# Kernel tuning notes

Measured on AMD Instinct MI355X. Metric: run time of the kernel, lower is better.

Reference implementation:

```python
import jax, jax.numpy as jnp
import numpy as np

HIDDEN = 2048
HEADS = 16
HEAD_DIM = HIDDEN // HEADS  # 128
B, S = 2, 2048
SCALE = 1.0 / np.sqrt(HEAD_DIM)


def setup_inputs() -> dict:
    key = jax.random.key(0)
    ks = jax.random.split(key, 9)
    x = jax.random.normal(ks[0], (B, S, HIDDEN), dtype=jnp.float32)
    # causal mask, broadcastable to [B, 1(group), H, S, S]
    mask = jnp.tril(jnp.ones((S, S), dtype=bool))[None, None, None, :, :]
    mask = jnp.broadcast_to(mask, (B, 1, 1, S, S))
    s = 0.02
    Wq = jax.random.normal(ks[1], (HIDDEN, HIDDEN), dtype=jnp.float32) * s
    bq = jnp.zeros((HIDDEN,), dtype=jnp.float32)
    Wk = jax.random.normal(ks[2], (HIDDEN, HEAD_DIM), dtype=jnp.float32) * s
    bk = jnp.zeros((HEAD_DIM,), dtype=jnp.float32)
    Wv = jax.random.normal(ks[3], (HIDDEN, HEAD_DIM), dtype=jnp.float32) * s
    bv = jnp.zeros((HEAD_DIM,), dtype=jnp.float32)
    Wo = jax.random.normal(ks[4], (HIDDEN, HIDDEN), dtype=jnp.float32) * s
    bo = jnp.zeros((HIDDEN,), dtype=jnp.float32)
    return {"x": x, "mask": mask, "Wq": Wq, "bq": bq, "Wk": Wk, "bk": bk,
            "Wv": Wv, "bv": bv, "Wo": Wo, "bo": bo}


def reference(x, mask, Wq, bq, Wk, bk, Wv, bv, Wo, bo):
    b, s, _ = x.shape
    q = (x @ Wq + bq).reshape(b, s, HEADS, HEAD_DIM)   # [b,s,h,d]
    k = x @ Wk + bk                                    # [b,t,d] single shared KV head
    v = x @ Wv + bv                                    # [b,t,d]
    # scores: [b, h, s, t]; add group dim to match mask [b,1,h,s,t]
    scores = jnp.einsum('bshd,btd->bhst', q, k) * SCALE
    scores = scores[:, None]                            # [b,1,h,s,t]
    scores = jnp.where(mask, scores, jnp.float32(-jnp.inf))
    att = jax.nn.softmax(scores, axis=-1)[:, 0]         # [b,h,s,t] (dropout eval = identity)
    out = jnp.einsum('bhst,btd->bshd', att, v).reshape(b, s, HIDDEN)
    return out @ Wo + bo
```

## Files before the change

### kernel.cpp

```cpp
#include <hip/hip_runtime.h>


#define HIDDEN 2048
#define NHEADS 16
#define HDIM 128
#define BATCH 2
#define SEQ 2048
#define SCALE_L2E 0.1275258653864023f

typedef __attribute__((ext_vector_type(8))) short bfrag;
typedef __attribute__((ext_vector_type(4))) float facc;

__device__ __forceinline__ unsigned short f2bf(float f) {
  unsigned int u = __float_as_uint(f);
  u += 0x7fffu + ((u >> 16) & 1u);
  return (unsigned short)(u >> 16);
}

__device__ __forceinline__ unsigned int cvt_pk_bf16(float lo, float hi) {
  unsigned int r;
  asm("v_cvt_pk_bf16_f32 %0, %1, %2" : "=v"(r) : "v"(lo), "v"(hi));
  return r;
}

__device__ __forceinline__ void gl_lds16(const void* g, void* l) {
  __builtin_amdgcn_global_load_lds(
      (const __attribute__((address_space(1))) void*)g,
      (__attribute__((address_space(3))) void*)l, 16, 0, 0);
}

__global__ __launch_bounds__(256) void cvt_bf16(const float* __restrict__ in,
                                                unsigned int* __restrict__ out, int n4) {
  int i = blockIdx.x * 256 + threadIdx.x;
  if (i >= n4) return;
  float4 v = ((const float4*)in)[i];
  uint2 o = {cvt_pk_bf16(v.x, v.y), cvt_pk_bf16(v.z, v.w)};
  ((uint2*)out)[i] = o;
}

__global__ __launch_bounds__(256) void transpose_cvt2(const float* __restrict__ W0,
                                                      short* __restrict__ T0,
                                                      const float* __restrict__ W1,
                                                      short* __restrict__ T1,
                                                      int K, int N) {
  const float* W = blockIdx.z ? W1 : W0;
  short* WT = blockIdx.z ? T1 : T0;
  __shared__ float t[32][33];
  int tx = threadIdx.x & 31, ty = threadIdx.x >> 5;
  int n0 = blockIdx.x * 32, k0 = blockIdx.y * 32;
#pragma unroll
  for (int j = 0; j < 4; ++j)
    t[ty + j * 8][tx] = W[(size_t)(k0 + ty + j * 8) * N + n0 + tx];
  __syncthreads();
#pragma unroll
  for (int j = 0; j < 4; ++j)
    WT[(size_t)(n0 + ty + j * 8) * K + k0 + tx] = (short)f2bf(t[tx][ty + j * 8]);
}

#define GEMM_STAGE8(buf, kt, A, BT, Kdim)                                      \
  _Pragma("unroll") for (int it_ = 0; it_ < 2; ++it_) {                        \
    int bc = (w * 2 + it_) * 64;                                               \
    int C = bc + l;                                                            \
    int row = C >> 3, c = C & 7;                                               \
    int gofs = (kt) * 64 + ((c ^ (row & 7)) << 3);                             \
    gl_lds16((A) + (size_t)(m0 + row) * (Kdim) + gofs, &Al[buf][bc * 8]);      \
    gl_lds16((BT) + (size_t)(n0 + row) * (Kdim) + gofs, &Bl[buf][bc * 8]);     \
  }

#define GEMM_PIPE_LOOP8(A, BT, Kdim)                                           \
  facc acc[2][4] = {};                                                         \
  const int nkt = (Kdim) >> 6;                                                 \
  GEMM_STAGE8(0, 0, A, BT, Kdim)                                               \
  __syncthreads();                                                             \
  for (int kt = 0; kt < nkt; ++kt) {                                           \
    const int cur = kt & 1;                                                    \
    if (kt + 1 < nkt) { GEMM_STAGE8(cur ^ 1, kt + 1, A, BT, Kdim) }            \
    __builtin_amdgcn_s_setprio(1);                                             \
    _Pragma("unroll") for (int ks = 0; ks < 2; ++ks) {                         \
      bfrag af[2], bf[4];                                                      \
      _Pragma("unroll") for (int mt = 0; mt < 2; ++mt) {                       \
        int row = wm * 32 + mt * 16 + l15;                                     \
        int c = ks * 4 + l4;                                                   \
        af[mt] = *(const bfrag*)&Al[cur][row * 64 + ((c ^ (row & 7)) << 3)];   \
      }                                                                        \
      _Pragma("unroll") for (int nt = 0; nt < 4; ++nt) {                       \
        int row = wn * 64 + nt * 16 + l15;                                     \
        int c = ks * 4 + l4;                                                   \
        bf[nt] = *(const bfrag*)&Bl[cur][row * 64 + ((c ^ (row & 7)) << 3)];   \
      }                                                                        \
      _Pragma("unroll") for (int mt = 0; mt < 2; ++mt)                         \
          _Pragma("unroll") for (int nt = 0; nt < 4; ++nt)                     \
              acc[mt][nt] = __builtin_amdgcn_mfma_f32_16x16x32_bf16(           \
                  af[mt], bf[nt], acc[mt][nt], 0, 0, 0);                       \
    }                                                                          \
    __builtin_amdgcn_s_setprio(0);                                             \
    __syncthreads();                                                           \
  }

__global__ __launch_bounds__(512, 4) void gemm_qkv(const short* __restrict__ A,
                                                   const short* __restrict__ BT,
                                                   const float* __restrict__ bq,
                                                   const float* __restrict__ bk,
                                                   const float* __restrict__ bv,
                                                   unsigned short* __restrict__ Qb,
                                                   unsigned short* __restrict__ Kb,
                                                   unsigned short* __restrict__ Vtb,
                                                   int M, int K) {
  __shared__ __align__(16) short Al[2][128 * 64];
  __shared__ __align__(16) short Bl[2][128 * 64];
  const int tid = threadIdx.x;
  const int w = tid >> 6, l = tid & 63;
  const int wm = w >> 1, wn = w & 1;
  const int l15 = l & 15, l4 = l >> 4;
  const int m0 = blockIdx.x * 128, n0 = blockIdx.y * 128;
  GEMM_PIPE_LOOP8(A, BT, K)
#pragma unroll
  for (int mt = 0; mt < 2; ++mt) {
#pragma unroll
    for (int nt = 0; nt < 4; ++nt) {
#pragma unroll
      for (int r = 0; r < 4; ++r) {
        int row = m0 + wm * 32 + mt * 16 + l4 * 4 + r;
        int col = n0 + wn * 64 + nt * 16 + l15;
        float v = acc[mt][nt][r];
        if (col < HIDDEN) {
          Qb[(size_t)row * HIDDEN + col] = f2bf(v + bq[col]);
        } else if (col < HIDDEN + HDIM) {
          int lc = col - HIDDEN;
          Kb[(size_t)row * HDIM + lc] = f2bf(v + bk[lc]);
        } else {
          int lc = col - HIDDEN - HDIM;
          Vtb[(size_t)lc * M + row] = f2bf(v + bv[lc]);
        }
      }
    }
  }
}

__global__ __launch_bounds__(512, 4) void gemm_out(const short* __restrict__ A,
                                                   const short* __restrict__ BT,
                                                   const float* __restrict__ bias,
                                                   float* __restrict__ Cout,
                                                   int M, int N, int K) {
  __shared__ __align__(16) short Al[2][128 * 64];
  __shared__ __align__(16) short Bl[2][128 * 64];
  const int tid = threadIdx.x;
  const int w = tid >> 6, l = tid & 63;
  const int wm = w >> 1, wn = w & 1;
  const int l15 = l & 15, l4 = l >> 4;
  const int m0 = blockIdx.x * 128, n0 = blockIdx.y * 128;
  GEMM_PIPE_LOOP8(A, BT, K)
#pragma unroll
  for (int mt = 0; mt < 2; ++mt)
#pragma unroll
    for (int nt = 0; nt < 4; ++nt)
#pragma unroll
      for (int r = 0; r < 4; ++r) {
        int row = m0 + wm * 32 + mt * 16 + l4 * 4 + r;
        int col = n0 + wn * 64 + nt * 16 + l15;
        Cout[(size_t)row * N + col] = acc[mt][nt][r] + bias[col];
      }
}

__global__ __launch_bounds__(256, 2) void attn_kernel(const short* __restrict__ Q,
                                                      const short* __restrict__ Kg,
                                                      const short* __restrict__ Vt,
                                                      unsigned short* __restrict__ O) {
  __shared__ __align__(16) short Kl[2][64 * 128];
  __shared__ __align__(16) short Vl[2][128 * 64];
  __shared__ __align__(16) char Pl[4][2048];
  const int tid = threadIdx.x;
  const int w = tid >> 6, l = tid & 63;
  const int l15 = l & 15, l4 = l >> 4;
  const int h = blockIdx.y, b = blockIdx.z;

#define STAGE_KV(buf, t)                                                            \
  do {                                                                              \
    const int kv0_ = (t) << 6;                                                      \
    _Pragma("unroll") for (int it = 0; it < 4; ++it) {                              \
      int bc = (w * 4 + it) * 64;                                                   \
      int C = bc + l;                                                               \
      int key = C >> 4, c = C & 15;                                                 \
      gl_lds16(Kg + (size_t)(b * SEQ + kv0_ + key) * HDIM + ((c ^ (key & 7)) << 3), \
               &Kl[buf][bc * 8]);                                                   \
    }                                                                               \
    _Pragma("unroll") for (int it = 0; it < 4; ++it) {                              \
      int bc = (w * 4 + it) * 64;                                                   \
      int C = bc + l;                                                               \
      int d = C >> 3, c = C & 7;                                                    \
      gl_lds16(Vt + (size_t)d * (BATCH * SEQ) + b * SEQ + kv0_ + ((c ^ (d & 7)) << 3), \
               &Vl[buf][bc * 8]);                                                   \
    }                                                                               \
  } while (0)

  for (int pass = 0; pass < 2; ++pass) {
    const int qtile = (pass == 0) ? (int)blockIdx.x : 31 - (int)blockIdx.x;
    const int q0 = qtile * 64;
    const int qw = q0 + w * 16;

    bfrag aq[4];
#pragma unroll
    for (int kk = 0; kk < 4; ++kk)
      aq[kk] = *(const bfrag*)(Q + (size_t)(b * SEQ + qw + l15) * HIDDEN +
                               h * HDIM + kk * 32 + l4 * 8);

    facc accO[8] = {};
    float mrow = -INFINITY, lrow = 0.f;
    const int nkv = qtile + 1;

    STAGE_KV(0, 0);
    __syncthreads();

    for (int t = 0; t < nkv; ++t) {
      const int cur = t & 1;
      if (t + 1 < nkv) STAGE_KV(cur ^ 1, t + 1);
      const int kv0 = t << 6;

      facc sac[4] = {};
      __builtin_amdgcn_s_setprio(1);
#pragma unroll
      for (int kk = 0; kk < 4; ++kk) {
        int c = kk * 4 + l4;
#pragma unroll
        for (int kt = 0; kt < 4; ++kt) {
          int key = kt * 16 + l15;
          bfrag ak = *(const bfrag*)&Kl[cur][key * 128 + ((c ^ (key & 7)) << 3)];
          sac[kt] = __builtin_amdgcn_mfma_f32_16x16x32_bf16(ak, aq[kk], sac[kt], 0, 0, 0);
        }
      }
      __builtin_amdgcn_s_setprio(0);

      const int qg = qw + l15;
      const bool needmask = (kv0 + 63 > qw);
      float p[4][4];
      float mt = -INFINITY;
#pragma unroll
      for (int kt = 0; kt < 4; ++kt)
#pragma unroll
        for (int r = 0; r < 4; ++r) {
          float v = sac[kt][r] * SCALE_L2E;
          if (needmask) {
            int keyg = kv0 + kt * 16 + l4 * 4 + r;
            v = (keyg <= qg) ? v : -INFINITY;
          }
          p[kt][r] = v;
          mt = fmaxf(mt, v);
        }
      mt = fmaxf(mt, __shfl_xor(mt, 16));
      mt = fmaxf(mt, __shfl_xor(mt, 32));
      float mn = fmaxf(mrow, mt);
      float f = exp2f(mrow - mn);
      mrow = mn;
      float ps = 0.f;
#pragma unroll
      for (int kt = 0; kt < 4; ++kt)
#pragma unroll
        for (int r = 0; r < 4; ++r) {
          p[kt][r] = exp2f(p[kt][r] - mn);
          ps += p[kt][r];
        }
      ps += __shfl_xor(ps, 16);
      ps += __shfl_xor(ps, 32);
      lrow = lrow * f + ps;
      float fr[4];
#pragma unroll
      for (int r = 0; r < 4; ++r) fr[r] = __shfl(f, l4 * 4 + r);

      char* pw = &Pl[w][0];
#pragma unroll
      for (int kt = 0; kt < 4; ++kt)
#pragma unroll
        for (int rp = 0; rp < 2; ++rp) {
          unsigned int u = cvt_pk_bf16(p[kt][2 * rp], p[kt][2 * rp + 1]);
          int byte = (l15 * 128 + (kt * 16 + l4 * 4 + 2 * rp) * 2) ^ ((l15 & 7) << 4);
          *(unsigned int*)(pw + byte) = u;
        }
#pragma unroll
      for (int nt = 0; nt < 8; ++nt)
#pragma unroll
        for (int r = 0; r < 4; ++r) accO[nt][r] *= fr[r];

      __builtin_amdgcn_s_setprio(1);
#pragma unroll
      for (int kc = 0; kc < 2; ++kc) {
        bfrag pa = *(const bfrag*)(&Pl[w][0] +
                                   ((l15 * 128 + (kc * 32 + l4 * 8) * 2) ^ ((l15 & 7) << 4)));
#pragma unroll
        for (int nt = 0; nt < 8; ++nt) {
          int d = nt * 16 + l15;
          int cslot = (kc * 4 + l4) ^ (d & 7);
          bfrag bv = *(const bfrag*)&Vl[cur][d * 64 + (cslot << 3)];
          accO[nt] = __builtin_amdgcn_mfma_f32_16x16x32_bf16(pa, bv, accO[nt], 0, 0, 0);
        }
      }
      __builtin_amdgcn_s_setprio(0);
      __syncthreads();
    }

    float inv = 1.f / lrow;
#pragma unroll
    for (int r = 0; r < 4; ++r) {
      float invr = __shfl(inv, l4 * 4 + r);
      int row = qw + l4 * 4 + r;
#pragma unroll
      for (int nt = 0; nt < 8; ++nt)
        O[(size_t)(b * SEQ + row) * HIDDEN + h * HDIM + nt * 16 + l15] =
            f2bf(accO[nt][r] * invr);
    }
  }
#undef STAGE_KV
}

extern "C" void kernel_launch(void* const* d_in, const int* in_sizes, int n_in,
                              void* d_out, int out_size, void* d_ws, size_t ws_size,
                              hipStream_t stream) {
  const float* x = (const float*)d_in[0];
  const float* Wq = (const float*)d_in[2];
  const float* bq = (const float*)d_in[3];
  const float* Wk = (const float*)d_in[4];
  const float* bk = (const float*)d_in[5];
  const float* Wv = (const float*)d_in[6];
  const float* bv = (const float*)d_in[7];
  const float* Wo = (const float*)d_in[8];
  const float* bo = (const float*)d_in[9];
  float* out = (float*)d_out;

  const size_t MS = (size_t)BATCH * SEQ;
  char* ws = (char*)d_ws;
  short* xb = (short*)ws;      ws += MS * HIDDEN * 2;
  short* WqkvT = (short*)ws;   ws += (size_t)(HIDDEN + 2 * HDIM) * HIDDEN * 2;
  short* WoT = (short*)ws;     ws += (size_t)HIDDEN * HIDDEN * 2;
  short* Qb = (short*)ws;      ws += MS * HIDDEN * 2;
  short* Kb = (short*)ws;      ws += MS * HDIM * 2;
  short* Vtb = (short*)ws;     ws += (size_t)HDIM * MS * 2;
  short* Ab = (short*)ws;      ws += MS * HIDDEN * 2;

  cvt_bf16<<<(int)(MS * HIDDEN / 4 / 256), 256, 0, stream>>>(
      x, (unsigned int*)xb, (int)(MS * HIDDEN / 4));
  transpose_cvt2<<<dim3(HIDDEN / 32, HIDDEN / 32, 2), 256, 0, stream>>>(
      Wq, WqkvT, Wo, WoT, HIDDEN, HIDDEN);
  transpose_cvt2<<<dim3(HDIM / 32, HIDDEN / 32, 2), 256, 0, stream>>>(
      Wk, WqkvT + (size_t)HIDDEN * HIDDEN, Wv, WqkvT + (size_t)(HIDDEN + HDIM) * HIDDEN,
      HIDDEN, HDIM);

  gemm_qkv<<<dim3(32, 18), 512, 0, stream>>>(xb, WqkvT, bq, bk, bv,
                                             (unsigned short*)Qb, (unsigned short*)Kb,
                                             (unsigned short*)Vtb, (int)MS, HIDDEN);

  attn_kernel<<<dim3(16, NHEADS, BATCH), 256, 0, stream>>>(Qb, Kb, Vtb,
                                                           (unsigned short*)Ab);

  gemm_out<<<dim3(32, 16), 512, 0, stream>>>(Ab, WoT, bo, out, (int)MS, HIDDEN, HIDDEN);
}
```

Before: 211.6 us.

## Keep P in registers, fold softmax scale into Wq, add lazy rescaling

Removes the per-wave LDS round trip for the probability tile by packing P straight into MFMA A-operand registers and reading V with a permuted key layout that matches it. The softmax scale times log2e is folded into the Wq weights and bq bias during conversion, so no multiply on scores is needed. The running max and output rescale are skipped unless some row's max grows by more than 8 (log2 units). This trades extra V fragment registers (16 bfrags) and possible occupancy pressure for less LDS traffic and ALU work. The threshold bounds exp values by 2^8, which may affect bf16 precision.

```diff
diff --git a/kernel.cpp b/kernel.cpp
--- a/kernel.cpp
+++ b/kernel.cpp
@@ -9,7 +9,9 @@
 #define SCALE_L2E 0.1275258653864023f
 
 typedef __attribute__((ext_vector_type(8))) short bfrag;
+typedef __attribute__((ext_vector_type(4))) short bhalf;
 typedef __attribute__((ext_vector_type(4))) float facc;
+typedef __attribute__((ext_vector_type(4))) unsigned int uifrag;
 
 __device__ __forceinline__ unsigned short f2bf(float f) {
   unsigned int u = __float_as_uint(f);
@@ -42,9 +44,11 @@
                                                       short* __restrict__ T0,
                                                       const float* __restrict__ W1,
                                                       short* __restrict__ T1,
-                                                      int K, int N) {
+                                                      int K, int N,
+                                                      float s0, float s1) {
   const float* W = blockIdx.z ? W1 : W0;
   short* WT = blockIdx.z ? T1 : T0;
+  const float s = blockIdx.z ? s1 : s0;
   __shared__ float t[32][33];
   int tx = threadIdx.x & 31, ty = threadIdx.x >> 5;
   int n0 = blockIdx.x * 32, k0 = blockIdx.y * 32;
@@ -54,7 +58,7 @@
   __syncthreads();
 #pragma unroll
   for (int j = 0; j < 4; ++j)
-    WT[(size_t)(n0 + ty + j * 8) * K + k0 + tx] = (short)f2bf(t[tx][ty + j * 8]);
+    WT[(size_t)(n0 + ty + j * 8) * K + k0 + tx] = (short)f2bf(t[tx][ty + j * 8] * s);
 }
 
 #define GEMM_STAGE8(buf, kt, A, BT, Kdim)                                      \
@@ -124,7 +128,7 @@
         int col = n0 + wn * 64 + nt * 16 + l15;
         float v = acc[mt][nt][r];
         if (col < HIDDEN) {
-          Qb[(size_t)row * HIDDEN + col] = f2bf(v + bq[col]);
+          Qb[(size_t)row * HIDDEN + col] = f2bf(v + bq[col] * SCALE_L2E);
         } else if (col < HIDDEN + HDIM) {
           int lc = col - HIDDEN;
           Kb[(size_t)row * HDIM + lc] = f2bf(v + bk[lc]);
@@ -168,7 +172,6 @@
                                                       unsigned short* __restrict__ O) {
   __shared__ __align__(16) short Kl[2][64 * 128];
   __shared__ __align__(16) short Vl[2][128 * 64];
-  __shared__ __align__(16) char Pl[4][2048];
   const int tid = threadIdx.x;
   const int w = tid >> 6, l = tid & 63;
   const int l15 = l & 15, l4 = l >> 4;
@@ -230,68 +233,79 @@
       }
       __builtin_amdgcn_s_setprio(0);
 
+      bfrag bv[16];
+#pragma unroll
+      for (int c = 0; c < 2; ++c)
+#pragma unroll
+        for (int nt = 0; nt < 8; ++nt) {
+          int d = nt * 16 + l15;
+          int cc = c * 4 + (l4 >> 1);
+          int base = d * 64 + (l4 & 1) * 4;
+          bhalf lo = *(const bhalf*)&Vl[cur][base + ((cc ^ (d & 7)) << 3)];
+          bhalf hi = *(const bhalf*)&Vl[cur][base + (((cc + 2) ^ (d & 7)) << 3)];
+          bv[c * 8 + nt] = __builtin_shufflevector(lo, hi, 0, 1, 2, 3, 4, 5, 6, 7);
+        }
+
       const int qg = qw + l15;
       const bool needmask = (kv0 + 63 > qw);
       float p[4][4];
-      float mt = -INFINITY;
 #pragma unroll
       for (int kt = 0; kt < 4; ++kt)
 #pragma unroll
         for (int r = 0; r < 4; ++r) {
-          float v = sac[kt][r] * SCALE_L2E;
+          float v = sac[kt][r];
           if (needmask) {
             int keyg = kv0 + kt * 16 + l4 * 4 + r;
             v = (keyg <= qg) ? v : -INFINITY;
           }
           p[kt][r] = v;
-          mt = fmaxf(mt, v);
         }
+      float m0_ = fmaxf(fmaxf(p[0][0], p[0][1]), fmaxf(p[0][2], p[0][3]));
+      float m1_ = fmaxf(fmaxf(p[1][0], p[1][1]), fmaxf(p[1][2], p[1][3]));
+      float m2_ = fmaxf(fmaxf(p[2][0], p[2][1]), fmaxf(p[2][2], p[2][3]));
+      float m3_ = fmaxf(fmaxf(p[3][0], p[3][1]), fmaxf(p[3][2], p[3][3]));
+      float mt = fmaxf(fmaxf(m0_, m1_), fmaxf(m2_, m3_));
       mt = fmaxf(mt, __shfl_xor(mt, 16));
       mt = fmaxf(mt, __shfl_xor(mt, 32));
-      float mn = fmaxf(mrow, mt);
-      float f = exp2f(mrow - mn);
-      mrow = mn;
-      float ps = 0.f;
+      if (!__all(mt <= mrow + 8.0f)) {
+        float mn = fmaxf(mrow, mt);
+        float f = exp2f(mrow - mn);
+        mrow = mn;
+        lrow *= f;
+        float fr[4];
+#pragma unroll
+        for (int r = 0; r < 4; ++r) fr[r] = __shfl(f, l4 * 4 + r);
+#pragma unroll
+        for (int nt = 0; nt < 8; ++nt)
+#pragma unroll
+          for (int r = 0; r < 4; ++r) accO[nt][r] *= fr[r];
+      }
 #pragma unroll
       for (int kt = 0; kt < 4; ++kt)
 #pragma unroll
-        for (int r = 0; r < 4; ++r) {
-          p[kt][r] = exp2f(p[kt][r] - mn);
-          ps += p[kt][r];
-        }
+        for (int r = 0; r < 4; ++r) p[kt][r] = exp2f(p[kt][r] - mrow);
+      float s0_ = (p[0][0] + p[0][1]) + (p[0][2] + p[0][3]);
+      float s1_ = (p[1][0] + p[1][1]) + (p[1][2] + p[1][3]);
+      float s2_ = (p[2][0] + p[2][1]) + (p[2][2] + p[2][3]);
+      float s3_ = (p[3][0] + p[3][1]) + (p[3][2] + p[3][3]);
+      float ps = (s0_ + s1_) + (s2_ + s3_);
       ps += __shfl_xor(ps, 16);
       ps += __shfl_xor(ps, 32);
-      lrow = lrow * f + ps;
-      float fr[4];
-#pragma unroll
-      for (int r = 0; r < 4; ++r) fr[r] = __shfl(f, l4 * 4 + r);
-
-      char* pw = &Pl[w][0];
-#pragma unroll
-      for (int kt = 0; kt < 4; ++kt)
-#pragma unroll
-        for (int rp = 0; rp < 2; ++rp) {
-          unsigned int u = cvt_pk_bf16(p[kt][2 * rp], p[kt][2 * rp + 1]);
-          int byte = (l15 * 128 + (kt * 16 + l4 * 4 + 2 * rp) * 2) ^ ((l15 & 7) << 4);
-          *(unsigned int*)(pw + byte) = u;
-        }
-#pragma unroll
-      for (int nt = 0; nt < 8; ++nt)
-#pragma unroll
-        for (int r = 0; r < 4; ++r) accO[nt][r] *= fr[r];
+      lrow += ps;
 
       __builtin_amdgcn_s_setprio(1);
 #pragma unroll
-      for (int kc = 0; kc < 2; ++kc) {
-        bfrag pa = *(const bfrag*)(&Pl[w][0] +
-                                   ((l15 * 128 + (kc * 32 + l4 * 8) * 2) ^ ((l15 & 7) << 4)));
-#pragma unroll
-        for (int nt = 0; nt < 8; ++nt) {
-          int d = nt * 16 + l15;
-          int cslot = (kc * 4 + l4) ^ (d & 7);
-          bfrag bv = *(const bfrag*)&Vl[cur][d * 64 + (cslot << 3)];
-          accO[nt] = __builtin_amdgcn_mfma_f32_16x16x32_bf16(pa, bv, accO[nt], 0, 0, 0);
-        }
+      for (int c = 0; c < 2; ++c) {
+        uifrag up;
+        up.x = cvt_pk_bf16(p[2 * c][0], p[2 * c][1]);
+        up.y = cvt_pk_bf16(p[2 * c][2], p[2 * c][3]);
+        up.z = cvt_pk_bf16(p[2 * c + 1][0], p[2 * c + 1][1]);
+        up.w = cvt_pk_bf16(p[2 * c + 1][2], p[2 * c + 1][3]);
+        bfrag pa = __builtin_bit_cast(bfrag, up);
+#pragma unroll
+        for (int nt = 0; nt < 8; ++nt)
+          accO[nt] = __builtin_amdgcn_mfma_f32_16x16x32_bf16(pa, bv[c * 8 + nt],
+                                                             accO[nt], 0, 0, 0);
       }
       __builtin_amdgcn_s_setprio(0);
       __syncthreads();
@@ -338,10 +352,10 @@
   cvt_bf16<<<(int)(MS * HIDDEN / 4 / 256), 256, 0, stream>>>(
       x, (unsigned int*)xb, (int)(MS * HIDDEN / 4));
   transpose_cvt2<<<dim3(HIDDEN / 32, HIDDEN / 32, 2), 256, 0, stream>>>(
-      Wq, WqkvT, Wo, WoT, HIDDEN, HIDDEN);
+      Wq, WqkvT, Wo, WoT, HIDDEN, HIDDEN, SCALE_L2E, 1.0f);
   transpose_cvt2<<<dim3(HDIM / 32, HIDDEN / 32, 2), 256, 0, stream>>>(
       Wk, WqkvT + (size_t)HIDDEN * HIDDEN, Wv, WqkvT + (size_t)(HIDDEN + HDIM) * HIDDEN,
-      HIDDEN, HDIM);
+      HIDDEN, HDIM, 1.0f, 1.0f);
 
   gemm_qkv<<<dim3(32, 18), 512, 0, stream>>>(xb, WqkvT, bq, bk, bv,
                                              (unsigned short*)Qb, (unsigned short*)Kb,
```

After: 222.2 us. 1.05x slower.
